# Optimization experiments

Measured on AMD Instinct MI355X. Metric: run time of the kernel, lower is better.

The kernel has to match this reference:

```python
import jax, jax.numpy as jnp
import numpy as np

N_SRC, N_DST, E, D, H = 100000, 10000, 320000, 128, 128
LN_EPS = 1e-5


def setup_inputs() -> dict:
    key = jax.random.key(0)
    ks = jax.random.split(key, 12)
    h_src = jax.random.normal(ks[0], (N_SRC, D), jnp.float32)
    h_dst = jax.random.normal(ks[1], (N_DST, D), jnp.float32)
    s_emb = jax.random.normal(ks[2], (N_DST, D), jnp.float32)
    edge_weight = jax.random.uniform(ks[3], (E,), jnp.float32)
    src_idx = jax.random.randint(ks[4], (E,), 0, N_SRC)
    dst_idx = jnp.sort(jax.random.randint(ks[5], (E,), 0, N_DST))
    # session_attention: Linear(2D->H, no bias) -> tanh -> Linear(H->1, no bias)
    W1 = jax.random.normal(ks[6], (2 * D, H), jnp.float32) / np.sqrt(2 * D)
    w2 = jax.random.normal(ks[7], (H,), jnp.float32) / np.sqrt(H)
    # output_proj: Linear(2D->D) with bias
    Wo = jax.random.normal(ks[8], (2 * D, D), jnp.float32) / np.sqrt(2 * D)
    bo = jnp.zeros((D,), jnp.float32)
    gamma = jnp.ones((D,), jnp.float32)
    beta = jnp.zeros((D,), jnp.float32)
    return {"h_src": h_src, "h_dst": h_dst, "s_emb": s_emb,
            "edge_weight": edge_weight, "src_idx": src_idx, "dst_idx": dst_idx,
            "W1": W1, "w2": w2, "Wo": Wo, "bo": bo, "gamma": gamma, "beta": beta}


def reference(h_src, h_dst, s_emb, edge_weight, src_idx, dst_idx, W1, w2, Wo, bo, gamma, beta):
    d = h_src.shape[1]
    # concat([h_src[src], s_emb[dst]]) @ W1 == h_src[src] @ W1[:d] + s_emb[dst] @ W1[d:]
    # project per-node first (cheaper than per-edge concat matmul)
    p_src = h_src @ W1[:d]          # [N_src, H]
    p_dst = s_emb @ W1[d:]          # [N_dst, H]
    raw = jnp.tanh(p_src[src_idx] + p_dst[dst_idx]) @ w2   # [E]
    raw = raw * edge_weight
    # edge_softmax: segment softmax over incoming edges of each dst node
    seg_max = jax.ops.segment_max(raw, dst_idx, num_segments=h_dst.shape[0])
    seg_max = jnp.where(jnp.isfinite(seg_max), seg_max, 0.0)  # handle degree-0 dsts
    ex = jnp.exp(raw - seg_max[dst_idx])
    den = jax.ops.segment_sum(ex, dst_idx, num_segments=h_dst.shape[0])
    attn = ex / den[dst_idx]                                 # [E]
    # u_mul_e + sum: weighted gather-scatter aggregation
    h_global = jax.ops.segment_sum(h_src[src_idx] * attn[:, None], dst_idx,
                                   num_segments=h_dst.shape[0])  # [N_dst, D]
    # output_proj on concat([h_dst, h_global])
    out = h_dst @ Wo[:d] + h_global @ Wo[d:] + bo
    # residual + layer norm (dropout = identity in eval)
    x = h_dst + out
    mu = jnp.mean(x, axis=-1, keepdims=True)
    var = jnp.mean((x - mu) ** 2, axis=-1, keepdims=True)
    y = (x - mu) / jnp.sqrt(var + LN_EPS) * gamma + beta
    return (y, attn[:, None])
```

## Files before the change

### kernel.cpp

```cpp
#include <hip/hip_runtime.h>
#include <math.h>

#define D128 128
#define SCAPW 256

typedef unsigned int uint32;
typedef unsigned short ushort_t;
typedef short bf16x8 __attribute__((ext_vector_type(8)));
typedef float f32x4 __attribute__((ext_vector_type(4)));
typedef float f32x2 __attribute__((ext_vector_type(2)));

__device__ __forceinline__ ushort_t bf16_of(float x) {
  uint32 u = __float_as_uint(x);
  return (ushort_t)((u + 0x7fffu + ((u >> 16) & 1u)) >> 16);
}
__device__ __forceinline__ uint32 pack_bf2(float x, float y) {
  uint32 bx = __float_as_uint(x);
  uint32 by = __float_as_uint(y);
  bx = (bx + 0x7fffu + ((bx >> 16) & 1u)) >> 16;
  by = (by + 0x7fffu + ((by >> 16) & 1u)) & 0xffff0000u;
  return bx | by;
}

__device__ __forceinline__ float fast_tanh(float x) {
  float e = __expf(2.0f * x);
  float r = __builtin_amdgcn_rcpf(1.0f + e);
  return fmaf(-2.0f, r, 1.0f);
}

__device__ __forceinline__ uint32 pack_fp8x4(float a, float b, float c, float d) {
  int u = __builtin_amdgcn_cvt_pk_fp8_f32(a, b, 0, false);
  u = __builtin_amdgcn_cvt_pk_fp8_f32(c, d, u, true);
  return (uint32)u;
}

__device__ __forceinline__ bf16x8 bf16x8_of(float4 a, float4 c) {
  union { uint4 u; bf16x8 h; } r;
  r.u.x = pack_bf2(a.x, a.y);
  r.u.y = pack_bf2(a.z, a.w);
  r.u.z = pack_bf2(c.x, c.y);
  r.u.w = pack_bf2(c.z, c.w);
  return r.h;
}

__device__ __forceinline__ void gload_lds16(const void* g, void* l) {
  __builtin_amdgcn_global_load_lds(
      (const __attribute__((address_space(1))) unsigned int*)g,
      (__attribute__((address_space(3))) unsigned int*)l, 16, 0, 0);
}

__device__ __forceinline__ float score8(uint2 us, f32x2 pd0, f32x2 pd1, f32x2 pd2,
                                        f32x2 pd3, float4 wA, float4 wB) {
  f32x2 a0 = __builtin_amdgcn_cvt_pk_f32_fp8(us.x, false);
  f32x2 a1 = __builtin_amdgcn_cvt_pk_f32_fp8(us.x, true);
  f32x2 a2 = __builtin_amdgcn_cvt_pk_f32_fp8(us.y, false);
  f32x2 a3 = __builtin_amdgcn_cvt_pk_f32_fp8(us.y, true);
  float sc;
  sc = fast_tanh(a0.x + pd0.x) * wA.x;
  sc = fmaf(fast_tanh(a0.y + pd0.y), wA.y, sc);
  sc = fmaf(fast_tanh(a1.x + pd1.x), wA.z, sc);
  sc = fmaf(fast_tanh(a1.y + pd1.y), wA.w, sc);
  sc = fmaf(fast_tanh(a2.x + pd2.x), wB.x, sc);
  sc = fmaf(fast_tanh(a2.y + pd2.y), wB.y, sc);
  sc = fmaf(fast_tanh(a3.x + pd3.x), wB.z, sc);
  sc = fmaf(fast_tanh(a3.y + pd3.y), wB.w, sc);
  return sc;
}

__global__ __launch_bounds__(256) void prep_all(
    const float* __restrict__ W1, const float* __restrict__ Wo,
    const int* __restrict__ dst_idx,
    ushort_t* __restrict__ Wfrag, ushort_t* __restrict__ Wo_frag,
    int* __restrict__ off, int E, int N) {
  const int b = blockIdx.x;
  const int tid = threadIdx.x;
  if (b < 16) {
    int t = b * 256 + tid;
    int lane = t & 63;
    int kc = (t >> 6) & 3;
    int nt = (t >> 8) & 7;
    int h = (t >> 11) & 1;
    int m = lane & 15;
    int quad = lane >> 4;
    int krow = h * D128 + kc * 32 + quad * 8;
    int ncol = nt * 16 + m;
    ushort_t fr[8];
#pragma unroll
    for (int j = 0; j < 8; j++) fr[j] = bf16_of(W1[(size_t)(krow + j) * D128 + ncol]);
    *(uint4*)(Wfrag + (size_t)t * 8) = *(const uint4*)fr;
  } else if (b < 32) {
    int t = (b - 16) * 256 + tid;
    int lane = t & 63;
    int kc = (t >> 6) & 7;
    int nt = (t >> 9) & 7;
    int m = lane & 15;
    int quad = lane >> 4;
    int krow = kc * 32 + quad * 8;
    int ncol = nt * 16 + m;
    ushort_t fr[8];
#pragma unroll
    for (int j = 0; j < 8; j++) fr[j] = bf16_of(Wo[(size_t)(krow + j) * D128 + ncol]);
    *(uint4*)(Wo_frag + (size_t)t * 8) = *(const uint4*)fr;
  } else {
    int e = (b - 32) * 256 + tid;
    if (e >= E) return;
    int d = dst_idx[e];
    int dprev = (e == 0) ? -1 : dst_idx[e - 1];
    for (int v = dprev + 1; v <= d; v++) off[v] = e;
    if (e == E - 1) {
      for (int v = d + 1; v <= N; v++) off[v] = E;
    }
  }
}

__global__ __launch_bounds__(256) void gemm_mfma(
    const float* __restrict__ Xa, const float* __restrict__ Xb,
    const ushort_t* __restrict__ Wfrag,
    uint32* __restrict__ Pa, uint32* __restrict__ Pb,
    uint32* __restrict__ x_f8,
    int Ma, int Mb, int nblk_a) {
  __shared__ uint4 WL[2048];
  const int blk = blockIdx.x;
  const float* X;
  const uint4* Wg;
  uint32* P;
  int M, row0;
  bool emit8;
  if (blk < nblk_a) {
    X = Xa; P = Pa; Wg = (const uint4*)Wfrag;             M = Ma; row0 = blk * 64; emit8 = true;
  } else {
    X = Xb; P = Pb; Wg = (const uint4*)(Wfrag + 16384);   M = Mb; row0 = (blk - nblk_a) * 64; emit8 = false;
  }

  const int tid = threadIdx.x;
  const int wave = tid >> 6;
  const int lane = tid & 63;
  const int m = lane & 15;
  const int quad = lane >> 4;

#pragma unroll
  for (int j = 0; j < 8; j++)
    gload_lds16(Wg + tid + 256 * j, &WL[(tid & ~63) + 256 * j]);

  const int ra = min(row0 + wave * 16 + m, M - 1);
  const float* xp = X + (size_t)ra * D128 + quad * 8;

  float4 xf[8];
#pragma unroll
  for (int kc = 0; kc < 4; kc++) {
    xf[kc * 2]     = *(const float4*)(xp + kc * 32);
    xf[kc * 2 + 1] = *(const float4*)(xp + kc * 32 + 4);
  }

  if (emit8) {
#pragma unroll
    for (int kc = 0; kc < 4; kc++) {
      uint2 q;
      q.x = pack_fp8x4(xf[kc * 2].x, xf[kc * 2].y, xf[kc * 2].z, xf[kc * 2].w);
      q.y = pack_fp8x4(xf[kc * 2 + 1].x, xf[kc * 2 + 1].y, xf[kc * 2 + 1].z, xf[kc * 2 + 1].w);
      *(uint2*)(x_f8 + (size_t)ra * 32 + kc * 8 + quad * 2) = q;
    }
  }
  bf16x8 xb[4];
#pragma unroll
  for (int kc = 0; kc < 4; kc++) xb[kc] = bf16x8_of(xf[kc * 2], xf[kc * 2 + 1]);

  __syncthreads();

  f32x4 acc[8];
#pragma unroll
  for (int nt = 0; nt < 8; nt++) acc[nt] = (f32x4){0.f, 0.f, 0.f, 0.f};

#pragma unroll
  for (int kc = 0; kc < 4; kc++) {
#pragma unroll
    for (int nt = 0; nt < 8; nt++) {
      bf16x8 wf = *(const bf16x8*)&WL[(nt * 4 + kc) * 64 + lane];
      acc[nt] = __builtin_amdgcn_mfma_f32_16x16x32_bf16(wf, xb[kc], acc[nt], 0, 0, 0);
    }
  }

  __syncthreads();
  uint32* Ys = (uint32*)WL;
#pragma unroll
  for (int nt = 0; nt < 8; nt++)
    Ys[(wave * 16 + m) * 36 + nt * 4 + quad] =
        pack_fp8x4(acc[nt][0], acc[nt][1], acc[nt][2], acc[nt][3]);
  __syncthreads();

#pragma unroll
  for (int it = 0; it < 2; it++) {
    int f = tid + 256 * it;
    int row = f >> 3;
    int cu = (f & 7) * 4;
    int grow = row0 + row;
    if (grow < M) *(uint4*)(P + (size_t)grow * 32 + cu) = *(const uint4*)(&Ys[row * 36 + cu]);
  }
}

__global__ __launch_bounds__(256) void attn_agg_kernel(
    const uint32* __restrict__ p_src_f8, const uint32* __restrict__ p_dst_f8,
    const float* __restrict__ w2, const float* __restrict__ ew,
    const int* __restrict__ src_idx, const int* __restrict__ off,
    const uint32* __restrict__ h_src_f8,
    float* __restrict__ attn_out, uint32* __restrict__ h_glob_bf, int N_dst) {
  const int tid = threadIdx.x;
  const int wv = tid >> 6;
  const int lane = tid & 63;
  const int v = blockIdx.x * 4 + wv;

  __shared__ float sex[4][SCAPW];
  __shared__ int ssrc[4][SCAPW];
  __shared__ float sew[4][SCAPW];
  if (v >= N_dst) return;

  const int lo = off[v], hi = off[v + 1];
  const int deg = hi - lo;
  const int sub = lane & 15;
  const int eg = lane >> 4;
  const bool fast = (deg <= SCAPW);

  float4 wA = *(const float4*)(w2 + sub * 8);
  float4 wB = *(const float4*)(w2 + sub * 8 + 4);
  uint2 pdu = *(const uint2*)(p_dst_f8 + (size_t)v * 32 + sub * 2);
  f32x2 pd0 = __builtin_amdgcn_cvt_pk_f32_fp8(pdu.x, false);
  f32x2 pd1 = __builtin_amdgcn_cvt_pk_f32_fp8(pdu.x, true);
  f32x2 pd2 = __builtin_amdgcn_cvt_pk_f32_fp8(pdu.y, false);
  f32x2 pd3 = __builtin_amdgcn_cvt_pk_f32_fp8(pdu.y, true);

  float den = 0.f;

  if (fast) {
    for (int i = lane; i < deg; i += 64) {
      ssrc[wv][i] = src_idx[lo + i];
      sew[wv][i] = ew[lo + i];
    }
    for (int base = 0; base < deg; base += 16) {
      int ei[4], ss[4];
      float ewv[4];
      uint2 us[4];
      bool vl[4];
#pragma unroll
      for (int j = 0; j < 4; j++) {
        ei[j] = base + j * 4 + eg;
        vl[j] = ei[j] < deg;
        const int ii = vl[j] ? ei[j] : 0;
        ss[j] = ssrc[wv][ii];
        ewv[j] = sew[wv][ii];
        us[j] = *(const uint2*)(p_src_f8 + (size_t)ss[j] * 32 + sub * 2);
      }
#pragma unroll
      for (int j = 0; j < 4; j++) {
        if (!vl[j]) continue;
        float sc = score8(us[j], pd0, pd1, pd2, pd3, wA, wB);
#pragma unroll
        for (int o = 1; o <= 8; o <<= 1) sc += __shfl_xor(sc, o, 64);
        float e = __expf(sc * ewv[j]);
        if (sub == 0) sex[wv][ei[j]] = e;
        den += (sub == 0) ? e : 0.f;
      }
    }
  } else {
    for (int base = 0; base < deg; base += 8) {
      const int ei0 = base + eg;
      const int ei1 = base + 4 + eg;
      const bool v0 = ei0 < deg;
      const bool v1 = ei1 < deg;
      int s0 = 0, s1 = 0;
      float ew0 = 0.f, ew1 = 0.f;
      uint2 us0, us1;
      us0.x = us0.y = us1.x = us1.y = 0u;
      if (v0) {
        const int e = lo + ei0;
        s0 = src_idx[e];
        ew0 = ew[e];
        us0 = *(const uint2*)(p_src_f8 + (size_t)s0 * 32 + sub * 2);
      }
      if (v1) {
        const int e = lo + ei1;
        s1 = src_idx[e];
        ew1 = ew[e];
        us1 = *(const uint2*)(p_src_f8 + (size_t)s1 * 32 + sub * 2);
      }
      float ex0 = 0.f, ex1 = 0.f;
      if (v0) {
        float sc = score8(us0, pd0, pd1, pd2, pd3, wA, wB);
#pragma unroll
        for (int o = 1; o <= 8; o <<= 1) sc += __shfl_xor(sc, o, 64);
        ex0 = __expf(sc * ew0);
        if (sub == 0) attn_out[lo + ei0] = ex0;
      }
      if (v1) {
        float sc = score8(us1, pd0, pd1, pd2, pd3, wA, wB);
#pragma unroll
        for (int o = 1; o <= 8; o <<= 1) sc += __shfl_xor(sc, o, 64);
        ex1 = __expf(sc * ew1);
        if (sub == 0) attn_out[lo + ei1] = ex1;
      }
      den += (sub == 0) ? (ex0 + ex1) : 0.f;
    }
  }
#pragma unroll
  for (int o = 1; o <= 32; o <<= 1) den += __shfl_xor(den, o, 64);
  const float inv = (deg > 0) ? 1.0f / den : 0.0f;

  const int c4 = lane & 31;
  const int hw = lane >> 5;
  float a0 = 0.f, a1 = 0.f, a2 = 0.f, a3 = 0.f;

  if (fast) {
    const int pad = (deg + 15) & ~15;
    for (int i = deg + lane; i < pad; i += 64) { sex[wv][i] = 0.f; ssrc[wv][i] = 0; }
    for (int i = lane; i < deg; i += 64) attn_out[lo + i] = sex[wv][i] * inv;
    for (int b = 0; b < pad; b += 16) {
#pragma unroll
      for (int j = 0; j < 8; j++) {
        const int idx = b + j * 2 + hw;
        float ex = sex[wv][idx];
        int s = ssrc[wv][idx];
        uint32 u = h_src_f8[(size_t)s * 32 + c4];
        f32x2 h0 = __builtin_amdgcn_cvt_pk_f32_fp8(u, false);
        f32x2 h1 = __builtin_amdgcn_cvt_pk_f32_fp8(u, true);
        a0 = fmaf(ex, h0.x, a0);
        a1 = fmaf(ex, h0.y, a1);
        a2 = fmaf(ex, h1.x, a2);
        a3 = fmaf(ex, h1.y, a3);
      }
    }
  } else {
    for (int b = 0; b < deg; b += 16) {
#pragma unroll
      for (int j = 0; j < 8; j++) {
        const int idx = b + j * 2 + hw;
        float ex = 0.f;
        int s = 0;
        if (idx < deg) { ex = attn_out[lo + idx]; s = src_idx[lo + idx]; }
        uint32 u = h_src_f8[(size_t)s * 32 + c4];
        f32x2 h0 = __builtin_amdgcn_cvt_pk_f32_fp8(u, false);
        f32x2 h1 = __builtin_amdgcn_cvt_pk_f32_fp8(u, true);
        a0 = fmaf(ex, h0.x, a0);
        a1 = fmaf(ex, h0.y, a1);
        a2 = fmaf(ex, h1.x, a2);
        a3 = fmaf(ex, h1.y, a3);
      }
    }
    for (int i = lane; i < deg; i += 64) attn_out[lo + i] *= inv;
  }

  a0 += __shfl_xor(a0, 32, 64);
  a1 += __shfl_xor(a1, 32, 64);
  a2 += __shfl_xor(a2, 32, 64);
  a3 += __shfl_xor(a3, 32, 64);
  if (hw == 0) {
    uint2 o;
    o.x = pack_bf2(a0 * inv, a1 * inv);
    o.y = pack_bf2(a2 * inv, a3 * inv);
    *(uint2*)(h_glob_bf + (size_t)v * 64 + c4 * 2) = o;
  }
}

__global__ __launch_bounds__(128) void out_mfma_ln(
    const float* __restrict__ h_dst, const ushort_t* __restrict__ h_glob_bf,
    const ushort_t* __restrict__ Wo_frag,
    const float* __restrict__ bo,
    const float* __restrict__ gamma, const float* __restrict__ beta,
    float* __restrict__ y, int N) {
  __shared__ uint4 WL[4096];
  const int tid = threadIdx.x;
  const int w = tid >> 6;
  const int lane = tid & 63;
  const int m = lane & 15;
  const int quad = lane >> 4;
  const int row0 = blockIdx.x * 32 + w * 16;
  const int ra = min(row0 + m, N - 1);
  const uint4* Wg = (const uint4*)Wo_frag;

#pragma unroll
  for (int j = 0; j < 32; j++)
    gload_lds16(Wg + tid + 128 * j, &WL[(tid & ~63) + 128 * j]);

  float4 f0[4], f1[4];
  bf16x8 ag[4];
#pragma unroll
  for (int kc = 0; kc < 4; kc++) {
    const float* p = h_dst + (size_t)ra * D128 + kc * 32 + quad * 8;
    f0[kc] = *(const float4*)p;
    f1[kc] = *(const float4*)(p + 4);
  }
#pragma unroll
  for (int kc = 0; kc < 4; kc++)
    ag[kc] = *(const bf16x8*)(h_glob_bf + (size_t)ra * D128 + kc * 32 + quad * 8);

  float bo_r[8], gm_r[8], bt_r[8];
#pragma unroll
  for (int nt = 0; nt < 8; nt++) {
    bo_r[nt] = bo[nt * 16 + m];
    gm_r[nt] = gamma[nt * 16 + m];
    bt_r[nt] = beta[nt * 16 + m];
  }

  __syncthreads();

  f32x4 acc[8];
#pragma unroll
  for (int nt = 0; nt < 8; nt++) acc[nt] = (f32x4){0.f, 0.f, 0.f, 0.f};

#pragma unroll
  for (int kc = 0; kc < 8; kc++) {
    bf16x8 a = (kc < 4) ? bf16x8_of(f0[kc & 3], f1[kc & 3]) : ag[kc & 3];
#pragma unroll
    for (int nt = 0; nt < 8; nt++) {
      bf16x8 bfr = *(const bf16x8*)&WL[(nt * 8 + kc) * 64 + lane];
      acc[nt] = __builtin_amdgcn_mfma_f32_16x16x32_bf16(a, bfr, acc[nt], 0, 0, 0);
    }
  }

#pragma unroll
  for (int r = 0; r < 4; r++) {
    const int grow = row0 + quad * 4 + r;
    const int gr = min(grow, N - 1);
    float x[8];
    float s1 = 0.f, s2 = 0.f;
#pragma unroll
    for (int nt = 0; nt < 8; nt++) {
      float hd = h_dst[(size_t)gr * D128 + nt * 16 + m];
      float xv = hd + acc[nt][r] + bo_r[nt];
      x[nt] = xv;
      s1 += xv;
      s2 = fmaf(xv, xv, s2);
    }
#pragma unroll
    for (int o = 1; o <= 8; o <<= 1) {
      s1 += __shfl_xor(s1, o, 64);
      s2 += __shfl_xor(s2, o, 64);
    }
    float mu = s1 * (1.0f / 128.0f);
    float var = s2 * (1.0f / 128.0f) - mu * mu;
    float rstd = __builtin_amdgcn_rcpf(sqrtf(var + 1e-5f));
    if (grow < N) {
#pragma unroll
      for (int nt = 0; nt < 8; nt++) {
        y[(size_t)grow * D128 + nt * 16 + m] = (x[nt] - mu) * rstd * gm_r[nt] + bt_r[nt];
      }
    }
  }
}

extern "C" void kernel_launch(void* const* d_in, const int* in_sizes, int n_in,
                              void* d_out, int out_size, void* d_ws, size_t ws_size,
                              hipStream_t stream) {
  const float* h_src = (const float*)d_in[0];
  const float* h_dst = (const float*)d_in[1];
  const float* s_emb = (const float*)d_in[2];
  const float* ew    = (const float*)d_in[3];
  const int* src_idx = (const int*)d_in[4];
  const int* dst_idx = (const int*)d_in[5];
  const float* W1    = (const float*)d_in[6];
  const float* w2    = (const float*)d_in[7];
  const float* Wo    = (const float*)d_in[8];
  const float* bo    = (const float*)d_in[9];
  const float* gamma = (const float*)d_in[10];
  const float* beta  = (const float*)d_in[11];

  const int N_src = in_sizes[0] / D128;
  const int N_dst = in_sizes[1] / D128;
  const int E = in_sizes[3];

  float* out_y = (float*)d_out;
  float* out_attn = out_y + (size_t)N_dst * D128;

  uint32* p_src_f8 = (uint32*)d_ws;
  uint32* p_dst_f8 = p_src_f8 + (size_t)N_src * 32;
  uint32* h_src_f8 = p_dst_f8 + (size_t)N_dst * 32;
  uint32* h_glob_bf = h_src_f8 + (size_t)N_src * 32;
  int* seg_off = (int*)(h_glob_bf + (size_t)N_dst * 64);
  ushort_t* Wfrag = (ushort_t*)(seg_off + N_dst + 1 + 3);
  ushort_t* Wo_frag = Wfrag + 32768;

  const int nblk_a = (N_src + 63) / 64;
  const int nblk_b = (N_dst + 63) / 64;
  const int nb_seg = (E + 255) / 256;

  prep_all<<<32 + nb_seg, 256, 0, stream>>>(
      W1, Wo, dst_idx, Wfrag, Wo_frag, seg_off, E, N_dst);
  gemm_mfma<<<nblk_a + nblk_b, 256, 0, stream>>>(
      h_src, s_emb, Wfrag, p_src_f8, p_dst_f8, h_src_f8, N_src, N_dst, nblk_a);
  attn_agg_kernel<<<(N_dst + 3) / 4, 256, 0, stream>>>(
      p_src_f8, p_dst_f8, w2, ew, src_idx, seg_off, h_src_f8, out_attn,
      h_glob_bf, N_dst);
  out_mfma_ln<<<(N_dst + 31) / 32, 128, 0, stream>>>(
      h_dst, (const ushort_t*)h_glob_bf, Wo_frag,
      bo, gamma, beta, out_y, N_dst);
}
```

Measured before the change: 157.8 us.

## Fuse score and aggregation passes in fast path to overlap gathers

In the low-degree fast path, the per-edge score/exp pass and the weighted h_src aggregation pass become one loop. The h_src fp8 rows for each 16-edge chunk are loaded alongside the p_src rows, and the unnormalized exp weights reach the aggregation lanes through shuffles. Normalization is still applied at the end. This removes a second sweep over the edges and lets the two gather streams overlap, at the cost of more registers per thread. tanh also now uses exp2 with a prescaled constant.

```diff
diff --git a/kernel.cpp b/kernel.cpp
--- a/kernel.cpp
+++ b/kernel.cpp
@@ -23,7 +23,7 @@
 }
 
 __device__ __forceinline__ float fast_tanh(float x) {
-  float e = __expf(2.0f * x);
+  float e = __builtin_exp2f(x * 2.8853900817779268f);
   float r = __builtin_amdgcn_rcpf(1.0f + e);
   return fmaf(-2.0f, r, 1.0f);
 }
@@ -218,6 +218,8 @@
   const int deg = hi - lo;
   const int sub = lane & 15;
   const int eg = lane >> 4;
+  const int c4 = lane & 31;
+  const int hw = lane >> 5;
   const bool fast = (deg <= SCAPW);
 
   float4 wA = *(const float4*)(w2 + sub * 8);
@@ -229,35 +231,54 @@
   f32x2 pd3 = __builtin_amdgcn_cvt_pk_f32_fp8(pdu.y, true);
 
   float den = 0.f;
+  float a0 = 0.f, a1 = 0.f, a2 = 0.f, a3 = 0.f;
 
   if (fast) {
+    const int pad = (deg + 15) & ~15;
     for (int i = lane; i < deg; i += 64) {
       ssrc[wv][i] = src_idx[lo + i];
       sew[wv][i] = ew[lo + i];
     }
-    for (int base = 0; base < deg; base += 16) {
-      int ei[4], ss[4];
+    for (int i = deg + lane; i < pad; i += 64) { ssrc[wv][i] = 0; sew[wv][i] = 0.f; }
+
+    for (int base = 0; base < pad; base += 16) {
+      uint2 us[4];
       float ewv[4];
-      uint2 us[4];
-      bool vl[4];
+      int ei[4];
 #pragma unroll
       for (int j = 0; j < 4; j++) {
         ei[j] = base + j * 4 + eg;
-        vl[j] = ei[j] < deg;
-        const int ii = vl[j] ? ei[j] : 0;
-        ss[j] = ssrc[wv][ii];
-        ewv[j] = sew[wv][ii];
-        us[j] = *(const uint2*)(p_src_f8 + (size_t)ss[j] * 32 + sub * 2);
-      }
+        int ss = ssrc[wv][ei[j]];
+        ewv[j] = sew[wv][ei[j]];
+        us[j] = *(const uint2*)(p_src_f8 + (size_t)ss * 32 + sub * 2);
+      }
+      uint32 uh[8];
+#pragma unroll
+      for (int t = 0; t < 8; t++) {
+        int s2 = ssrc[wv][base + 2 * t + hw];
+        uh[t] = h_src_f8[(size_t)s2 * 32 + c4];
+      }
+      float exj[4];
 #pragma unroll
       for (int j = 0; j < 4; j++) {
-        if (!vl[j]) continue;
         float sc = score8(us[j], pd0, pd1, pd2, pd3, wA, wB);
 #pragma unroll
         for (int o = 1; o <= 8; o <<= 1) sc += __shfl_xor(sc, o, 64);
-        float e = __expf(sc * ewv[j]);
+        float e = (ei[j] < deg) ? __expf(sc * ewv[j]) : 0.f;
+        exj[j] = e;
         if (sub == 0) sex[wv][ei[j]] = e;
         den += (sub == 0) ? e : 0.f;
+      }
+#pragma unroll
+      for (int t = 0; t < 8; t++) {
+        int srcl = ((((2 * t) & 3) + hw) << 4);
+        float exv = __shfl(exj[t >> 1], srcl, 64);
+        f32x2 h0 = __builtin_amdgcn_cvt_pk_f32_fp8(uh[t], false);
+        f32x2 h1 = __builtin_amdgcn_cvt_pk_f32_fp8(uh[t], true);
+        a0 = fmaf(exv, h0.x, a0);
+        a1 = fmaf(exv, h0.y, a1);
+        a2 = fmaf(exv, h1.x, a2);
+        a3 = fmaf(exv, h1.y, a3);
       }
     }
   } else {
@@ -304,29 +325,8 @@
   for (int o = 1; o <= 32; o <<= 1) den += __shfl_xor(den, o, 64);
   const float inv = (deg > 0) ? 1.0f / den : 0.0f;
 
-  const int c4 = lane & 31;
-  const int hw = lane >> 5;
-  float a0 = 0.f, a1 = 0.f, a2 = 0.f, a3 = 0.f;
-
   if (fast) {
-    const int pad = (deg + 15) & ~15;
-    for (int i = deg + lane; i < pad; i += 64) { sex[wv][i] = 0.f; ssrc[wv][i] = 0; }
     for (int i = lane; i < deg; i += 64) attn_out[lo + i] = sex[wv][i] * inv;
-    for (int b = 0; b < pad; b += 16) {
-#pragma unroll
-      for (int j = 0; j < 8; j++) {
-        const int idx = b + j * 2 + hw;
-        float ex = sex[wv][idx];
-        int s = ssrc[wv][idx];
-        uint32 u = h_src_f8[(size_t)s * 32 + c4];
-        f32x2 h0 = __builtin_amdgcn_cvt_pk_f32_fp8(u, false);
-        f32x2 h1 = __builtin_amdgcn_cvt_pk_f32_fp8(u, true);
-        a0 = fmaf(ex, h0.x, a0);
-        a1 = fmaf(ex, h0.y, a1);
-        a2 = fmaf(ex, h1.x, a2);
-        a3 = fmaf(ex, h1.y, a3);
-      }
-    }
   } else {
     for (int b = 0; b < deg; b += 16) {
 #pragma unroll
```

Measured after the change: 162.6 us. +3.0%, slower.
